# Optimization experiments

Hardware: AMD Instinct MI355X
Metric: run time of the kernel (lower is better)

## Reference

```python
import jax, jax.numpy as jnp
import numpy as np

D_MODEL = 1024
HEADS = 2
IDX_DIM = 32


def setup_inputs() -> dict:
    key = jax.random.key(0)
    kx, kq, kk, kw = jax.random.split(key, 4)
    x = jax.random.normal(kx, (2, 4096, D_MODEL), dtype=jnp.float32)
    # nn.Linear weights stored as [in, out] for direct x @ W
    scale = 1.0 / np.sqrt(D_MODEL)
    Wq = jax.random.normal(kq, (D_MODEL, HEADS * IDX_DIM), dtype=jnp.float32) * scale
    Wk = jax.random.normal(kk, (D_MODEL, IDX_DIM), dtype=jnp.float32) * scale
    Ww = jax.random.normal(kw, (D_MODEL, HEADS), dtype=jnp.float32) * scale
    return {"x": x, "Wq": Wq, "Wk": Wk, "Ww": Ww}


def reference(x, Wq, Wk, Ww):
    b, t, _ = x.shape
    queries = (x @ Wq).reshape(b, t, HEADS, IDX_DIM)   # [b,t,h,d]
    keys = x @ Wk                                       # [b,s,d]
    weights = x @ Ww                                    # [b,t,h]
    dots = jnp.einsum('bthd,bsd->bths', queries, keys)  # [b,t,h,s]
    activated = jax.nn.relu(dots)
    # per-head weight then reduce over heads -> [b,t,s]
    index_scores = jnp.einsum('bths,bth->bts', activated, weights)
    return index_scores
```

## Files before the change

### kernel.cpp

```cpp
#include <hip/hip_runtime.h>
#include <hip/hip_bf16.h>

#define DM    1024
#define NH    2
#define IDX   32
#define HQ    (NH*IDX)
#define TT    4096
#define BB    2
#define RR    (BB*TT)
#define NC    112
#define NTIL  7

typedef short  s16x8 __attribute__((ext_vector_type(8)));
typedef float  f32x4 __attribute__((ext_vector_type(4)));

__device__ __forceinline__ unsigned short f2bf(float f) {
    unsigned int u = __builtin_bit_cast(unsigned int, f);
    u += 0x7FFFu + ((u >> 16) & 1u);
    return (unsigned short)(u >> 16);
}

__global__ __launch_bounds__(256) void prep_wcat(const float* __restrict__ Wq,
                                                 const float* __restrict__ Wk,
                                                 const float* __restrict__ Ww,
                                                 unsigned short* __restrict__ WcatT) {
    int idx = blockIdx.x * 256 + threadIdx.x;
    int j = idx >> 10;
    int i = idx & 1023;
    float v = 0.f;
    if (j < 64)       v = Wq[i * HQ + j];
    else if (j < 96)  v = Wk[i * IDX + (j - 64)];
    else if (j < 98)  v = Ww[i * NH + (j - 96)];
    WcatT[j * DM + i] = f2bf(v);
}

__global__ __launch_bounds__(256) void proj_kernel(const float* __restrict__ x,
                                                   const unsigned short* __restrict__ WcatT,
                                                   unsigned short* __restrict__ Qb,
                                                   unsigned short* __restrict__ Kb,
                                                   float* __restrict__ wb) {
    __shared__ float red[2][NTIL][64][4];

    const int wave  = threadIdx.x >> 6;
    const int lane  = threadIdx.x & 63;
    const int sl    = wave >> 1;
    const int khalf = wave & 1;
    const int stripe = blockIdx.x * 2 + sl;
    const int r0    = stripe * 16;
    const int lrow  = lane & 15;
    const int lseg  = lane >> 4;

    f32x4 acc[NTIL] = {};

    const float*          xr = x + (size_t)(r0 + lrow) * DM + khalf * 512 + lseg * 8;
    const unsigned short* wr = WcatT + (size_t)lrow * DM + khalf * 512 + lseg * 8;

    #pragma unroll 2
    for (int kc = 0; kc < 512; kc += 32) {
        float4 a0 = *(const float4*)(xr + kc);
        float4 a1 = *(const float4*)(xr + kc + 4);
        s16x8 af;
        af[0] = (short)f2bf(a0.x); af[1] = (short)f2bf(a0.y);
        af[2] = (short)f2bf(a0.z); af[3] = (short)f2bf(a0.w);
        af[4] = (short)f2bf(a1.x); af[5] = (short)f2bf(a1.y);
        af[6] = (short)f2bf(a1.z); af[7] = (short)f2bf(a1.w);
        #pragma unroll
        for (int t = 0; t < NTIL; ++t) {
            s16x8 bfv = *(const s16x8*)(wr + (size_t)t * 16 * DM + kc);
            acc[t] = __builtin_amdgcn_mfma_f32_16x16x32_bf16(af, bfv, acc[t], 0, 0, 0);
        }
    }

    if (khalf == 1) {
        #pragma unroll
        for (int t = 0; t < NTIL; ++t)
            *(f32x4*)&red[sl][t][lane][0] = acc[t];
    }
    __syncthreads();
    if (khalf == 0) {
        #pragma unroll
        for (int t = 0; t < NTIL; ++t) {
            acc[t] += *(const f32x4*)&red[sl][t][lane][0];
            const int col = t * 16 + lrow;
            #pragma unroll
            for (int r = 0; r < 4; ++r) {
                int row = r0 + lseg * 4 + r;
                float v = acc[t][r];
                if (col < 64)       Qb[(size_t)row * HQ + col]         = f2bf(v);
                else if (col < 96)  Kb[(size_t)row * IDX + (col - 64)] = f2bf(v);
                else if (col < 98)  wb[(size_t)row * NH + (col - 96)]  = v;
            }
        }
    }
}

__global__ __launch_bounds__(256) void score_kernel(const unsigned short* __restrict__ Qb,
                                                    const unsigned short* __restrict__ Kb,
                                                    const float* __restrict__ wb,
                                                    float* __restrict__ out) {
    const int rb   = blockIdx.x >> 3;
    const int sc   = blockIdx.x & 7;
    const int wave = threadIdx.x >> 6;
    const int lane = threadIdx.x & 63;
    const int lrow = lane & 15;
    const int lseg = lane >> 4;

    const int t0 = rb * 64 + wave * 16;
    const int b  = t0 >> 12;

    const unsigned short* qrow = Qb + (size_t)(t0 + lrow) * HQ + lseg * 8;
    s16x8 qa0 = *(const s16x8*)(qrow);
    s16x8 qa1 = *(const s16x8*)(qrow + IDX);

    float2 wpair[4];
    #pragma unroll
    for (int r = 0; r < 4; ++r)
        wpair[r] = *(const float2*)(wb + (size_t)(t0 + lseg * 4 + r) * NH);

    const unsigned short* kbase =
        Kb + ((size_t)(b * TT) + sc * 512 + lrow) * IDX + lseg * 8;
    float* obase = out + (size_t)(t0 + lseg * 4) * TT + sc * 512 + lrow;

    const f32x4 zero = {0.f, 0.f, 0.f, 0.f};

    #pragma unroll 4
    for (int it = 0; it < 32; ++it) {
        s16x8 kb = *(const s16x8*)(kbase + (size_t)it * 16 * IDX);
        f32x4 d0 = __builtin_amdgcn_mfma_f32_16x16x32_bf16(qa0, kb, zero, 0, 0, 0);
        f32x4 d1 = __builtin_amdgcn_mfma_f32_16x16x32_bf16(qa1, kb, zero, 0, 0, 0);
        #pragma unroll
        for (int r = 0; r < 4; ++r) {
            float v = wpair[r].x * fmaxf(d0[r], 0.f)
                    + wpair[r].y * fmaxf(d1[r], 0.f);
            obase[(size_t)r * TT + it * 16] = v;
        }
    }
}

extern "C" void kernel_launch(void* const* d_in, const int* in_sizes, int n_in,
                              void* d_out, int out_size, void* d_ws, size_t ws_size,
                              hipStream_t stream) {
    const float* x  = (const float*)d_in[0];
    const float* Wq = (const float*)d_in[1];
    const float* Wk = (const float*)d_in[2];
    const float* Ww = (const float*)d_in[3];
    float* out = (float*)d_out;

    char* ws = (char*)d_ws;
    unsigned short* WcatT = (unsigned short*)ws;
    unsigned short* Qb    = (unsigned short*)(ws + 256 * 1024);
    unsigned short* Kb    = (unsigned short*)(ws + 256 * 1024 + 1024 * 1024);
    float*          wb    = (float*)(ws + 256 * 1024 + 1024 * 1024 + 512 * 1024);

    hipLaunchKernelGGL(prep_wcat, dim3((NC * DM) / 256), dim3(256), 0, stream,
                       Wq, Wk, Ww, WcatT);
    hipLaunchKernelGGL(proj_kernel, dim3(RR / 32), dim3(256), 0, stream,
                       x, WcatT, Qb, Kb, wb);
    hipLaunchKernelGGL(score_kernel, dim3((RR / 64) * 8), dim3(256), 0, stream,
                       Qb, Kb, wb, out);
}
```

Measured before the change: 51.91 us.

## Transpose score MFMA for vectorized float4 stores and split projection K four ways

The score kernel swaps the MFMA operand order so each lane owns one query row and four consecutive key columns. The output then goes out as a single float4 store per iteration instead of four strided scalar stores. It also shrinks the key chunk per block to 256, doubling the grid. The projection kernel now gives each block one 16-row stripe with four waves splitting K into quarters, reduced through shared memory, doubling that grid as well. The aim is better write coalescing on the dominant output store and more parallelism, at the cost of extra LDS reduction traffic.

```diff
diff --git a/kernel.cpp b/kernel.cpp
--- a/kernel.cpp
+++ b/kernel.cpp
@@ -10,6 +10,8 @@
 #define RR    (BB*TT)
 #define NC    112
 #define NTIL  7
+#define SCW   256
+#define SCH   (TT/SCW)
 
 typedef short  s16x8 __attribute__((ext_vector_type(8)));
 typedef float  f32x4 __attribute__((ext_vector_type(4)));
@@ -39,24 +41,21 @@
                                                    unsigned short* __restrict__ Qb,
                                                    unsigned short* __restrict__ Kb,
                                                    float* __restrict__ wb) {
-    __shared__ float red[2][NTIL][64][4];
+    __shared__ float red[3][NTIL][64][4];
 
-    const int wave  = threadIdx.x >> 6;
-    const int lane  = threadIdx.x & 63;
-    const int sl    = wave >> 1;
-    const int khalf = wave & 1;
-    const int stripe = blockIdx.x * 2 + sl;
-    const int r0    = stripe * 16;
-    const int lrow  = lane & 15;
-    const int lseg  = lane >> 4;
+    const int wave = threadIdx.x >> 6;
+    const int lane = threadIdx.x & 63;
+    const int r0   = blockIdx.x * 16;
+    const int lrow = lane & 15;
+    const int lseg = lane >> 4;
 
     f32x4 acc[NTIL] = {};
 
-    const float*          xr = x + (size_t)(r0 + lrow) * DM + khalf * 512 + lseg * 8;
-    const unsigned short* wr = WcatT + (size_t)lrow * DM + khalf * 512 + lseg * 8;
+    const float*          xr = x + (size_t)(r0 + lrow) * DM + wave * 256 + lseg * 8;
+    const unsigned short* wr = WcatT + (size_t)lrow * DM + wave * 256 + lseg * 8;
 
     #pragma unroll 2
-    for (int kc = 0; kc < 512; kc += 32) {
+    for (int kc = 0; kc < 256; kc += 32) {
         float4 a0 = *(const float4*)(xr + kc);
         float4 a1 = *(const float4*)(xr + kc + 4);
         s16x8 af;
@@ -71,16 +70,18 @@
         }
     }
 
-    if (khalf == 1) {
+    if (wave != 0) {
         #pragma unroll
         for (int t = 0; t < NTIL; ++t)
-            *(f32x4*)&red[sl][t][lane][0] = acc[t];
+            *(f32x4*)&red[wave - 1][t][lane][0] = acc[t];
     }
     __syncthreads();
-    if (khalf == 0) {
+    if (wave == 0) {
         #pragma unroll
         for (int t = 0; t < NTIL; ++t) {
-            acc[t] += *(const f32x4*)&red[sl][t][lane][0];
+            acc[t] += *(const f32x4*)&red[0][t][lane][0];
+            acc[t] += *(const f32x4*)&red[1][t][lane][0];
+            acc[t] += *(const f32x4*)&red[2][t][lane][0];
             const int col = t * 16 + lrow;
             #pragma unroll
             for (int r = 0; r < 4; ++r) {
@@ -98,42 +99,39 @@
                                                     const unsigned short* __restrict__ Kb,
                                                     const float* __restrict__ wb,
                                                     float* __restrict__ out) {
-    const int rb   = blockIdx.x >> 3;
-    const int sc   = blockIdx.x & 7;
+    const int rb   = blockIdx.x >> 4;
+    const int sc   = blockIdx.x & (SCH - 1);
     const int wave = threadIdx.x >> 6;
     const int lane = threadIdx.x & 63;
-    const int lrow = lane & 15;
+    const int trow = lane & 15;
     const int lseg = lane >> 4;
 
     const int t0 = rb * 64 + wave * 16;
     const int b  = t0 >> 12;
 
-    const unsigned short* qrow = Qb + (size_t)(t0 + lrow) * HQ + lseg * 8;
-    s16x8 qa0 = *(const s16x8*)(qrow);
-    s16x8 qa1 = *(const s16x8*)(qrow + IDX);
+    const unsigned short* qrow = Qb + (size_t)(t0 + trow) * HQ + lseg * 8;
+    s16x8 qb0 = *(const s16x8*)(qrow);
+    s16x8 qb1 = *(const s16x8*)(qrow + IDX);
 
-    float2 wpair[4];
-    #pragma unroll
-    for (int r = 0; r < 4; ++r)
-        wpair[r] = *(const float2*)(wb + (size_t)(t0 + lseg * 4 + r) * NH);
+    float2 wt = *(const float2*)(wb + (size_t)(t0 + trow) * NH);
 
+    const int s0 = sc * SCW;
     const unsigned short* kbase =
-        Kb + ((size_t)(b * TT) + sc * 512 + lrow) * IDX + lseg * 8;
-    float* obase = out + (size_t)(t0 + lseg * 4) * TT + sc * 512 + lrow;
+        Kb + ((size_t)(b * TT) + s0 + trow) * IDX + lseg * 8;
+    float* obase = out + (size_t)(t0 + trow) * TT + s0 + lseg * 4;
 
     const f32x4 zero = {0.f, 0.f, 0.f, 0.f};
 
     #pragma unroll 4
-    for (int it = 0; it < 32; ++it) {
+    for (int it = 0; it < SCW / 16; ++it) {
         s16x8 kb = *(const s16x8*)(kbase + (size_t)it * 16 * IDX);
-        f32x4 d0 = __builtin_amdgcn_mfma_f32_16x16x32_bf16(qa0, kb, zero, 0, 0, 0);
-        f32x4 d1 = __builtin_amdgcn_mfma_f32_16x16x32_bf16(qa1, kb, zero, 0, 0, 0);
+        f32x4 d0 = __builtin_amdgcn_mfma_f32_16x16x32_bf16(kb, qb0, zero, 0, 0, 0);
+        f32x4 d1 = __builtin_amdgcn_mfma_f32_16x16x32_bf16(kb, qb1, zero, 0, 0, 0);
+        f32x4 v;
         #pragma unroll
-        for (int r = 0; r < 4; ++r) {
-            float v = wpair[r].x * fmaxf(d0[r], 0.f)
-                    + wpair[r].y * fmaxf(d1[r], 0.f);
-            obase[(size_t)r * TT + it * 16] = v;
-        }
+        for (int r = 0; r < 4; ++r)
+            v[r] = wt.x * fmaxf(d0[r], 0.f) + wt.y * fmaxf(d1[r], 0.f);
+        *(f32x4*)(obase + it * 16) = v;
     }
 }
 
@@ -154,8 +152,8 @@
 
     hipLaunchKernelGGL(prep_wcat, dim3((NC * DM) / 256), dim3(256), 0, stream,
                        Wq, Wk, Ww, WcatT);
-    hipLaunchKernelGGL(proj_kernel, dim3(RR / 32), dim3(256), 0, stream,
+    hipLaunchKernelGGL(proj_kernel, dim3(RR / 16), dim3(256), 0, stream,
                        x, WcatT, Qb, Kb, wb);
-    hipLaunchKernelGGL(score_kernel, dim3((RR / 64) * 8), dim3(256), 0, stream,
+    hipLaunchKernelGGL(score_kernel, dim3((RR / 64) * SCH), dim3(256), 0, stream,
                        Qb, Kb, wb, out);
 }
```

Measured after the change: 55.51 us. +6.9%, slower.
